# Kernel optimization log

Measured on AMD Instinct MI355X. Metric: run time of the kernel, lower is better.

The kernel has to match this reference:

```python
import jax, jax.numpy as jnp
import numpy as np
from jax import lax

PATCH = 8

def setup_inputs() -> dict:
    key = jax.random.key(0)
    ks = jax.random.split(key, 5)
    x = jax.random.normal(ks[0], (4, 64, 256, 256), dtype=jnp.float32)
    w_in = jax.random.normal(ks[1], (512, 64), dtype=jnp.float32) * 0.02
    b_in = jnp.zeros((512,), dtype=jnp.float32)
    w_dw = jax.random.normal(ks[2], (512, 1, 3, 3), dtype=jnp.float32) * 0.02
    b_dw = jnp.zeros((512,), dtype=jnp.float32)
    w_out = jax.random.normal(ks[3], (64, 256), dtype=jnp.float32) * 0.02
    b_out = jnp.zeros((64,), dtype=jnp.float32)
    fft_filter = jnp.ones((64, 1, 1, PATCH, PATCH // 2 + 1), dtype=jnp.float32)
    return {"x": x, "w_in": w_in, "b_in": b_in, "w_dw": w_dw, "b_dw": b_dw,
            "w_out": w_out, "b_out": b_out, "fft_filter": fft_filter}

def reference(x, w_in, b_in, w_dw, b_dw, w_out, b_out, fft_filter):
    # project_in: 1x1 conv == channel GEMM. x: [B, C, H, W] -> [B, 2h, H, W]
    h = jnp.einsum('oc,bchw->bohw', w_in, x) + b_in[None, :, None, None]
    # depthwise 3x3 conv, padding=1
    h = lax.conv_general_dilated(
        h, w_dw, window_strides=(1, 1), padding='SAME',
        dimension_numbers=('NCHW', 'OIHW', 'NCHW'),
        feature_group_count=w_dw.shape[0]) + b_dw[None, :, None, None]
    x1, x2 = jnp.split(h, 2, axis=1)
    h = jax.nn.gelu(x1, approximate=False) * x2  # exact GELU like F.gelu
    # project_out: 1x1 conv
    y = jnp.einsum('oc,bchw->bohw', w_out, h) + b_out[None, :, None, None]
    # patch-wise spectral filtering
    B, C, H, W = y.shape
    p = PATCH
    yp = y.reshape(B, C, H // p, p, W // p, p).transpose(0, 1, 2, 4, 3, 5)  # b c h w p1 p2
    yf = jnp.fft.rfft2(yp)              # b c h w p1 (p2//2+1)
    yf = yf * fft_filter                # filter broadcasts over (c,1,1,p1,p2r)
    yp = jnp.fft.irfft2(yf, s=(p, p))
    y = yp.transpose(0, 1, 2, 4, 3, 5).reshape(B, C, H, W)
    return y
```

## Files before the change

### kernel.cpp

```cpp
#include <hip/hip_runtime.h>
#include <math.h>

typedef __attribute__((ext_vector_type(8))) short short8;
typedef __attribute__((ext_vector_type(4))) float f32x4;
typedef __attribute__((ext_vector_type(2))) float f32x2;

#define TX 16
#define TY 8
#define IH 256
#define IW 256

#define WSA_OFF 16384
#define WSC_OFF 81920

#define H_STRIDE 816
#define G_OFF 13056
#define SMEM_BYTES 21248

#define SP2(c) ((f32x2){(c), (c)})

__device__ __forceinline__ unsigned short f2bf(float f) {
  unsigned int u = __builtin_bit_cast(unsigned int, f);
  u = (u + 0x7FFFu + ((u >> 16) & 1u)) >> 16;
  return (unsigned short)u;
}
__device__ __forceinline__ float bflo(unsigned int v) {
  return __builtin_bit_cast(float, v << 16);
}
__device__ __forceinline__ float bfhi(unsigned int v) {
  return __builtin_bit_cast(float, v & 0xFFFF0000u);
}

__global__ void edffn_prep(const float* __restrict__ fftf,
                           const float* __restrict__ w_in,
                           const float* __restrict__ w_out,
                           float* __restrict__ ws) {
  int blk = blockIdx.x, t = threadIdx.x;
  if (blk < 64) {
    int a = t >> 3, bb = t & 7;
    const float c0 = 0.70710678118654752f;
    const float ctab[8] = {1.f, c0, 0.f, -c0, -1.f, -c0, 0.f, c0};
    const float* F = fftf + blk * 40;
    float acc = 0.f;
    for (int k1 = 0; k1 < 8; ++k1)
      for (int k2 = 0; k2 < 8; ++k2) {
        float f = (k2 <= 4) ? F[k1 * 5 + k2] : F[((8 - k1) & 7) * 5 + (8 - k2)];
        acc += f * ctab[(k1 * a + k2 * bb) & 7];
      }
    ws[blk * 64 + t] = acc * (1.f / 64.f);
  } else if (blk < 128) {
    int b2 = blk - 64;
    int q = b2 >> 2, s = (b2 >> 1) & 1, ks = b2 & 1;
    int row = (s ? 256 : 0) + q * 16 + (t & 15);
    unsigned short* dst =
        (unsigned short*)((unsigned char*)ws + WSA_OFF) + (((q * 2 + s) * 2 + ks) * 64 + t) * 8;
    for (int j = 0; j < 8; ++j) {
      int k = ks * 32 + (t >> 4) * 8 + j;
      dst[j] = f2bf(w_in[row * 64 + k]);
    }
  } else {
    int b3 = blk - 128;
    int p = b3 >> 2, mt = b3 & 3;
    int row = mt * 16 + (t & 15);
    unsigned short* dst =
        (unsigned short*)((unsigned char*)ws + WSC_OFF) + ((p * 4 + mt) * 64 + t) * 8;
    for (int j = 0; j < 8; ++j) {
      int k = p * 32 + (t >> 4) * 8 + j;
      dst[j] = f2bf(w_out[row * 256 + k]);
    }
  }
}

__global__ __launch_bounds__(256, 2) void edffn_main(
    const float* __restrict__ x, const float* __restrict__ b_in,
    const float* __restrict__ w_dw, const float* __restrict__ b_dw,
    const float* __restrict__ b_out, const float* __restrict__ ws,
    float* __restrict__ out) {
  __shared__ __align__(16) unsigned char smem[SMEM_BYTES];
  __shared__ int s_flag;
  const int t = threadIdx.x;
  const int lane = t & 63, wave = t >> 6;
  const int l15 = lane & 15, lg = lane >> 4;
  const int gx0 = blockIdx.x * TX, gy0 = blockIdx.y * TY;
  const int b = blockIdx.z;
  const unsigned short* wsA = (const unsigned short*)((const unsigned char*)ws + WSA_OFF);
  const unsigned short* wsC = (const unsigned short*)((const unsigned char*)ws + WSC_OFF);

  short8 xf[3][2];
  int haddr[3];
  unsigned vmask = 0, imask = 0;
  const float* xb = x + (size_t)b * 64 * 65536;
#pragma unroll
  for (int i = 0; i < 3; ++i) {
    int nt = wave + 4 * i;
    int n = nt * 16 + l15;
    int hy = n / 18;
    int hx = n - hy * 18;
    int gy = gy0 + hy - 1, gx = gx0 + hx - 1;
    int vnt = n < 180;
    int inb = vnt & (gy >= 0) & (gy < IH) & (gx >= 0) & (gx < IW);
    haddr[i] = hy * 80 + hx * 4;
    vmask |= (unsigned)vnt << i;
    imask |= (unsigned)inb << i;
    int gyc = min(max(gy, 0), IH - 1), gxc = min(max(gx, 0), IW - 1);
    const float* xp = xb + (size_t)gyc * IW + gxc;
#pragma unroll
    for (int ks = 0; ks < 2; ++ks) {
#pragma unroll
      for (int j = 0; j < 8; ++j) {
        int k = ks * 32 + lg * 8 + j;
        unsigned short bf = f2bf(xp[(size_t)k * 65536]);
        xf[i][ks][j] = (short)(inb ? bf : (unsigned short)0);
      }
    }
  }

  f32x4 accY[8];
#pragma unroll
  for (int i = 0; i < 8; ++i) accY[i] = (f32x4){0.f, 0.f, 0.f, 0.f};

  const int cp_dw = t >> 4;
  const int oy_dw = (t & 15) >> 1;
  const int h_dw = t & 1;

  for (int q = 0; q < 16; ++q) {
    {
      short8 af[2][2];
#pragma unroll
      for (int s = 0; s < 2; ++s)
#pragma unroll
        for (int ks = 0; ks < 2; ++ks)
          af[s][ks] = *(const short8*)(wsA + (((q * 2 + s) * 2 + ks) * 64 + lane) * 8);
      float bin[2][4];
#pragma unroll
      for (int s = 0; s < 2; ++s)
#pragma unroll
        for (int r = 0; r < 4; ++r) bin[s][r] = b_in[(s ? 256 : 0) + q * 16 + lg * 4 + r];
#pragma unroll
      for (int i = 0; i < 3; ++i) {
        f32x4 acc0 = {0.f, 0.f, 0.f, 0.f}, acc1 = {0.f, 0.f, 0.f, 0.f};
        acc0 = __builtin_amdgcn_mfma_f32_16x16x32_bf16(af[0][0], xf[i][0], acc0, 0, 0, 0);
        acc0 = __builtin_amdgcn_mfma_f32_16x16x32_bf16(af[0][1], xf[i][1], acc0, 0, 0, 0);
        acc1 = __builtin_amdgcn_mfma_f32_16x16x32_bf16(af[1][0], xf[i][0], acc1, 0, 0, 0);
        acc1 = __builtin_amdgcn_mfma_f32_16x16x32_bf16(af[1][1], xf[i][1], acc1, 0, 0, 0);
        if ((vmask >> i) & 1u) {
          unsigned keep = (imask >> i) & 1u;
#pragma unroll
          for (int r = 0; r < 4; ++r) {
            float v0 = acc0[r] + bin[0][r];
            float v1 = acc1[r] + bin[1][r];
            unsigned int pk;
            asm("v_cvt_pk_bf16_f32 %0, %1, %2" : "=v"(pk) : "v"(v0), "v"(v1));
            pk = keep ? pk : 0u;
            *(unsigned int*)(smem + (lg * 4 + r) * H_STRIDE + haddr[i]) = pk;
          }
        }
      }
    }
    __syncthreads();

    {
      const int cp = cp_dw, oy = oy_dw, h = h_dw;
      const int cg1 = q * 16 + cp, cg2 = 256 + q * 16 + cp;
      f32x2 wd[9];
#pragma unroll
      for (int u = 0; u < 9; ++u) wd[u] = (f32x2){w_dw[cg1 * 9 + u], w_dw[cg2 * 9 + u]};
      const f32x2 bd = (f32x2){b_dw[cg1], b_dw[cg2]};
      f32x2 a[8];
#pragma unroll
      for (int j = 0; j < 8; ++j) a[j] = bd;
#pragma unroll
      for (int dy = 0; dy < 3; ++dy) {
        const unsigned char* base = smem + cp * H_STRIDE + (oy + dy) * 80 + h * 32;
        uint4 r0 = *(const uint4*)base;
        uint4 r1 = *(const uint4*)(base + 16);
        uint2 r2 = *(const uint2*)(base + 32);
        f32x2 e[10];
#define UNP(ii, vv)                      \
  {                                      \
    unsigned int v_ = (vv);              \
    e[ii] = (f32x2){bflo(v_), bfhi(v_)}; \
  }
        UNP(0, r0.x) UNP(1, r0.y) UNP(2, r0.z) UNP(3, r0.w)
        UNP(4, r1.x) UNP(5, r1.y) UNP(6, r1.z) UNP(7, r1.w)
        UNP(8, r2.x) UNP(9, r2.y)
#undef UNP
#pragma unroll
        for (int ox = 0; ox < 8; ++ox) {
#pragma unroll
          for (int dx = 0; dx < 3; ++dx)
            a[ox] = __builtin_elementwise_fma(wd[dy * 3 + dx], e[ox + dx], a[ox]);
        }
      }
      const int c2 = (q & 1) * 16 + cp;
      const int gi = (c2 >> 3) ^ (oy & 3);
      unsigned short* Gp =
          (unsigned short*)(smem + G_OFF) + oy * 16 * 32 + gi * 8 + (c2 & 7);
#pragma unroll
      for (int j = 0; j < 4; ++j) {
        f32x2 u = (f32x2){a[2 * j][0], a[2 * j + 1][0]};
        f32x2 v = (f32x2){a[2 * j][1], a[2 * j + 1][1]};
        f32x2 z = u * 0.70710678118654752f;
        f32x2 z2 = z * z;
        f32x2 erfv;
        if (__builtin_expect(fmaxf(z2[0], z2[1]) > 0.16f, 0)) {
          erfv[0] = erff(z[0]);
          erfv[1] = erff(z[1]);
        } else {
          f32x2 p = __builtin_elementwise_fma(z2, SP2(1.f / 216.f), SP2(-1.f / 42.f));
          p = __builtin_elementwise_fma(z2, p, SP2(1.f / 10.f));
          p = __builtin_elementwise_fma(z2, p, SP2(-1.f / 3.f));
          p = __builtin_elementwise_fma(z2, p, SP2(1.f));
          erfv = 1.12837916709551257f * (z * p);
        }
        f32x2 tt = __builtin_elementwise_fma(erfv, SP2(0.5f), SP2(0.5f));
        f32x2 g = (u * tt) * v;
        Gp[(h * 8 + 2 * j) * 32] = f2bf(g[0]);
        Gp[(h * 8 + 2 * j + 1) * 32] = f2bf(g[1]);
      }
    }
    __syncthreads();

    if (q & 1) {
      const int p = q >> 1;
      short8 cf = *(const short8*)(wsC + ((p * 4 + wave) * 64 + lane) * 8);
      const unsigned short* G = (const unsigned short*)(smem + G_OFF);
#pragma unroll
      for (int nt = 0; nt < 8; ++nt) {
        int g = lg ^ (nt & 3);
        int n = nt * 16 + l15;
        short8 bf = *(const short8*)(G + n * 32 + g * 8);
        accY[nt] = __builtin_amdgcn_mfma_f32_16x16x32_bf16(cf, bf, accY[nt], 0, 0, 0);
      }
    }
  }

  {
    f32x4 bo;
#pragma unroll
    for (int r = 0; r < 4; ++r) bo[r] = b_out[wave * 16 + lg * 4 + r];
#pragma unroll
    for (int nt = 0; nt < 8; ++nt)
#pragma unroll
      for (int r = 0; r < 4; ++r) accY[nt][r] += bo[r];
  }

  if (t == 0) s_flag = 1;
  __syncthreads();
  {
    int ok = 1;
    const float* kc = ws;
#pragma unroll
    for (int j = 0; j < 16; ++j) {
      int idx = t * 16 + j;
      float e = ((idx & 63) == 0) ? 1.f : 0.f;
      ok &= (fabsf(kc[idx] - e) <= 1e-5f) ? 1 : 0;
    }
    if (!ok) s_flag = 0;
  }
  __syncthreads();

  const int o = wave * 16 + lg * 4;
  if (s_flag) {
#pragma unroll
    for (int nt = 0; nt < 8; ++nt) {
      float* op = out + (((size_t)(b * 64 + o)) * IH + gy0 + nt) * IW + gx0 + l15;
#pragma unroll
      for (int r = 0; r < 4; ++r) op[(size_t)r * IH * IW] = accY[nt][r];
    }
    return;
  }

  float* YS = (float*)smem;
  for (int half = 0; half < 2; ++half) {
    __syncthreads();
    if ((wave >> 1) == half) {
      int c32 = (wave & 1) * 16 + lg * 4;
#pragma unroll
      for (int nt = 0; nt < 8; ++nt)
#pragma unroll
        for (int r = 0; r < 4; ++r) YS[(c32 + r) * 132 + nt * 16 + l15] = accY[nt][r];
    }
    __syncthreads();
    if (t < 64) {
      int o32 = t >> 1, oo = half * 32 + o32, qd = t & 1;
      const float* kp = ws + oo * 64;
      int px0 = qd * 8;
      const float* row = YS + o32 * 132;
      for (int i = 0; i < 8; ++i)
        for (int j = 0; j < 8; ++j) {
          float acc = 0.f;
          for (int a_ = 0; a_ < 8; ++a_)
            for (int b_ = 0; b_ < 8; ++b_)
              acc += kp[a_ * 8 + b_] *
                     row[((i - a_) & 7) * 16 + px0 + ((j - b_) & 7)];
          out[(((size_t)(b * 64 + oo)) * IH + gy0 + i) * IW + gx0 + px0 + j] = acc;
        }
    }
  }
}

extern "C" void kernel_launch(void* const* d_in, const int* in_sizes, int n_in,
                              void* d_out, int out_size, void* d_ws, size_t ws_size,
                              hipStream_t stream) {
  const float* x = (const float*)d_in[0];
  const float* w_in = (const float*)d_in[1];
  const float* b_in = (const float*)d_in[2];
  const float* w_dw = (const float*)d_in[3];
  const float* b_dw = (const float*)d_in[4];
  const float* w_out = (const float*)d_in[5];
  const float* b_out = (const float*)d_in[6];
  const float* fftf = (const float*)d_in[7];
  float* out = (float*)d_out;
  float* ws = (float*)d_ws;

  edffn_prep<<<160, 64, 0, stream>>>(fftf, w_in, w_out, ws);
  dim3 grid(IW / TX, IH / TY, 4);
  edffn_main<<<grid, 256, 0, stream>>>(x, b_in, w_dw, b_dw, b_out, ws, out);
}
```

Baseline: 176.8 us.

## Prefetch next-iteration weights and store intermediate h tile in fp32 LDS

Software-pipelines the per-q weight loads (project_in A fragments, biases, depthwise weights, project_out fragments) so the next iteration's global loads are issued before the current compute, hiding their latency. The intermediate h tile in LDS is also switched from packed bf16 to fp32 pairs. This removes the bf16 pack/unpack work and gives the depthwise conv more precision. In exchange, LDS use roughly doubles, which may lower occupancy, and the prefetch buffers add register pressure.

After: 173.3 us. 2.0% less time.

```diff
diff --git a/kernel.cpp b/kernel.cpp
--- a/kernel.cpp
+++ b/kernel.cpp
@@ -13,9 +13,10 @@
 #define WSA_OFF 16384
 #define WSC_OFF 81920
 
-#define H_STRIDE 816
-#define G_OFF 13056
-#define SMEM_BYTES 21248
+#define H_ROWB 176
+#define H_PLANE 1760
+#define G_OFF 28160
+#define SMEM_BYTES 44544
 
 #define SP2(c) ((f32x2){(c), (c)})
 
@@ -23,12 +24,6 @@
   unsigned int u = __builtin_bit_cast(unsigned int, f);
   u = (u + 0x7FFFu + ((u >> 16) & 1u)) >> 16;
   return (unsigned short)u;
-}
-__device__ __forceinline__ float bflo(unsigned int v) {
-  return __builtin_bit_cast(float, v << 16);
-}
-__device__ __forceinline__ float bfhi(unsigned int v) {
-  return __builtin_bit_cast(float, v & 0xFFFF0000u);
 }
 
 __global__ void edffn_prep(const float* __restrict__ fftf,
@@ -99,7 +94,7 @@
     int gy = gy0 + hy - 1, gx = gx0 + hx - 1;
     int vnt = n < 180;
     int inb = vnt & (gy >= 0) & (gy < IH) & (gx >= 0) & (gx < IW);
-    haddr[i] = hy * 80 + hx * 4;
+    haddr[i] = hy * H_ROWB + hx * 8;
     vmask |= (unsigned)vnt << i;
     imask |= (unsigned)inb << i;
     int gyc = min(max(gy, 0), IH - 1), gxc = min(max(gx, 0), IW - 1);
@@ -123,36 +118,53 @@
   const int oy_dw = (t & 15) >> 1;
   const int h_dw = t & 1;
 
+  auto loadAF = [&](int qq, short8 (&af)[2][2], float (&bin)[2][4]) {
+#pragma unroll
+    for (int s = 0; s < 2; ++s) {
+#pragma unroll
+      for (int ks = 0; ks < 2; ++ks)
+        af[s][ks] = *(const short8*)(wsA + (((qq * 2 + s) * 2 + ks) * 64 + lane) * 8);
+#pragma unroll
+      for (int r = 0; r < 4; ++r) bin[s][r] = b_in[(s ? 256 : 0) + qq * 16 + lg * 4 + r];
+    }
+  };
+  auto loadWD = [&](int qq, f32x2 (&wd)[9], f32x2& bd) {
+    const int cg1 = qq * 16 + cp_dw, cg2 = 256 + qq * 16 + cp_dw;
+#pragma unroll
+    for (int u = 0; u < 9; ++u) wd[u] = (f32x2){w_dw[cg1 * 9 + u], w_dw[cg2 * 9 + u]};
+    bd = (f32x2){b_dw[cg1], b_dw[cg2]};
+  };
+
+  short8 afC[2][2], afN[2][2];
+  float binC[2][4], binN[2][4];
+  f32x2 wdC[9], wdN[9], bdC, bdN;
+  short8 cfC;
+
+  loadAF(0, afC, binC);
+  loadWD(0, wdC, bdC);
+  cfC = *(const short8*)(wsC + ((0 * 4 + wave) * 64 + lane) * 8);
+
   for (int q = 0; q < 16; ++q) {
+    if (q < 15) {
+      loadAF(q + 1, afN, binN);
+      loadWD(q + 1, wdN, bdN);
+    }
+
     {
-      short8 af[2][2];
-#pragma unroll
-      for (int s = 0; s < 2; ++s)
-#pragma unroll
-        for (int ks = 0; ks < 2; ++ks)
-          af[s][ks] = *(const short8*)(wsA + (((q * 2 + s) * 2 + ks) * 64 + lane) * 8);
-      float bin[2][4];
-#pragma unroll
-      for (int s = 0; s < 2; ++s)
-#pragma unroll
-        for (int r = 0; r < 4; ++r) bin[s][r] = b_in[(s ? 256 : 0) + q * 16 + lg * 4 + r];
 #pragma unroll
       for (int i = 0; i < 3; ++i) {
         f32x4 acc0 = {0.f, 0.f, 0.f, 0.f}, acc1 = {0.f, 0.f, 0.f, 0.f};
-        acc0 = __builtin_amdgcn_mfma_f32_16x16x32_bf16(af[0][0], xf[i][0], acc0, 0, 0, 0);
-        acc0 = __builtin_amdgcn_mfma_f32_16x16x32_bf16(af[0][1], xf[i][1], acc0, 0, 0, 0);
-        acc1 = __builtin_amdgcn_mfma_f32_16x16x32_bf16(af[1][0], xf[i][0], acc1, 0, 0, 0);
-        acc1 = __builtin_amdgcn_mfma_f32_16x16x32_bf16(af[1][1], xf[i][1], acc1, 0, 0, 0);
+        acc0 = __builtin_amdgcn_mfma_f32_16x16x32_bf16(afC[0][0], xf[i][0], acc0, 0, 0, 0);
+        acc0 = __builtin_amdgcn_mfma_f32_16x16x32_bf16(afC[0][1], xf[i][1], acc0, 0, 0, 0);
+        acc1 = __builtin_amdgcn_mfma_f32_16x16x32_bf16(afC[1][0], xf[i][0], acc1, 0, 0, 0);
+        acc1 = __builtin_amdgcn_mfma_f32_16x16x32_bf16(afC[1][1], xf[i][1], acc1, 0, 0, 0);
         if ((vmask >> i) & 1u) {
           unsigned keep = (imask >> i) & 1u;
 #pragma unroll
           for (int r = 0; r < 4; ++r) {
-            float v0 = acc0[r] + bin[0][r];
-            float v1 = acc1[r] + bin[1][r];
-            unsigned int pk;
-            asm("v_cvt_pk_bf16_f32 %0, %1, %2" : "=v"(pk) : "v"(v0), "v"(v1));
-            pk = keep ? pk : 0u;
-            *(unsigned int*)(smem + (lg * 4 + r) * H_STRIDE + haddr[i]) = pk;
+            f32x2 hv = (f32x2){acc0[r] + binC[0][r], acc1[r] + binC[1][r]};
+            if (!keep) hv = (f32x2){0.f, 0.f};
+            *(f32x2*)(smem + (lg * 4 + r) * H_PLANE + haddr[i]) = hv;
           }
         }
       }
@@ -161,35 +173,24 @@
 
     {
       const int cp = cp_dw, oy = oy_dw, h = h_dw;
-      const int cg1 = q * 16 + cp, cg2 = 256 + q * 16 + cp;
-      f32x2 wd[9];
-#pragma unroll
-      for (int u = 0; u < 9; ++u) wd[u] = (f32x2){w_dw[cg1 * 9 + u], w_dw[cg2 * 9 + u]};
-      const f32x2 bd = (f32x2){b_dw[cg1], b_dw[cg2]};
       f32x2 a[8];
 #pragma unroll
-      for (int j = 0; j < 8; ++j) a[j] = bd;
+      for (int j = 0; j < 8; ++j) a[j] = bdC;
 #pragma unroll
       for (int dy = 0; dy < 3; ++dy) {
-        const unsigned char* base = smem + cp * H_STRIDE + (oy + dy) * 80 + h * 32;
-        uint4 r0 = *(const uint4*)base;
-        uint4 r1 = *(const uint4*)(base + 16);
-        uint2 r2 = *(const uint2*)(base + 32);
+        const unsigned char* base = smem + cp * H_PLANE + (oy + dy) * H_ROWB + h * 64;
         f32x2 e[10];
-#define UNP(ii, vv)                      \
-  {                                      \
-    unsigned int v_ = (vv);              \
-    e[ii] = (f32x2){bflo(v_), bfhi(v_)}; \
-  }
-        UNP(0, r0.x) UNP(1, r0.y) UNP(2, r0.z) UNP(3, r0.w)
-        UNP(4, r1.x) UNP(5, r1.y) UNP(6, r1.z) UNP(7, r1.w)
-        UNP(8, r2.x) UNP(9, r2.y)
-#undef UNP
+#pragma unroll
+        for (int i5 = 0; i5 < 5; ++i5) {
+          f32x4 v = *(const f32x4*)(base + i5 * 16);
+          e[2 * i5] = (f32x2){v[0], v[1]};
+          e[2 * i5 + 1] = (f32x2){v[2], v[3]};
+        }
 #pragma unroll
         for (int ox = 0; ox < 8; ++ox) {
 #pragma unroll
           for (int dx = 0; dx < 3; ++dx)
-            a[ox] = __builtin_elementwise_fma(wd[dy * 3 + dx], e[ox + dx], a[ox]);
+            a[ox] = __builtin_elementwise_fma(wdC[dy * 3 + dx], e[ox + dx], a[ox]);
         }
       }
       const int c2 = (q & 1) * 16 + cp;
@@ -223,15 +224,29 @@
 
     if (q & 1) {
       const int p = q >> 1;
-      short8 cf = *(const short8*)(wsC + ((p * 4 + wave) * 64 + lane) * 8);
       const unsigned short* G = (const unsigned short*)(smem + G_OFF);
 #pragma unroll
       for (int nt = 0; nt < 8; ++nt) {
         int g = lg ^ (nt & 3);
         int n = nt * 16 + l15;
         short8 bf = *(const short8*)(G + n * 32 + g * 8);
-        accY[nt] = __builtin_amdgcn_mfma_f32_16x16x32_bf16(cf, bf, accY[nt], 0, 0, 0);
-      }
+        accY[nt] = __builtin_amdgcn_mfma_f32_16x16x32_bf16(cfC, bf, accY[nt], 0, 0, 0);
+      }
+      if (q < 15)
+        cfC = *(const short8*)(wsC + (((p + 1) * 4 + wave) * 64 + lane) * 8);
+    }
+
+    if (q < 15) {
+#pragma unroll
+      for (int s = 0; s < 2; ++s) {
+#pragma unroll
+        for (int ks = 0; ks < 2; ++ks) afC[s][ks] = afN[s][ks];
+#pragma unroll
+        for (int r = 0; r < 4; ++r) binC[s][r] = binN[s][r];
+      }
+#pragma unroll
+      for (int u = 0; u < 9; ++u) wdC[u] = wdN[u];
+      bdC = bdN;
     }
   }
 
```
